# Optimization experiments

Hardware: AMD Instinct MI355X
Metric: run time of the kernel (lower is better)

The kernel has to match this reference:

```python
import jax, jax.numpy as jnp
import numpy as np
import math

L, N, E, H = 2048, 4, 1024, 16  # seq_len, batch, embed_dim, num_heads
HD = E // H                      # head_dim = 64


def setup_inputs() -> dict:
    key = jax.random.key(0)
    ks = jax.random.split(key, 7)
    s = 1.0 / math.sqrt(E)
    return {
        "query": jax.random.normal(ks[0], (L, N, E), jnp.float32),
        "key": jax.random.normal(ks[1], (L, N, E), jnp.float32),
        "value": jax.random.normal(ks[2], (L, N, E), jnp.float32),
        "in_proj_weight": jax.random.normal(ks[3], (3 * E, E), jnp.float32) * s,
        "in_proj_bias": jax.random.normal(ks[4], (3 * E,), jnp.float32) * 0.02,
        "out_proj_weight": jax.random.normal(ks[5], (E, E), jnp.float32) * s,
        "out_proj_bias": jax.random.normal(ks[6], (E,), jnp.float32) * 0.02,
    }


def reference(query, key, value, in_proj_weight, in_proj_bias,
              out_proj_weight, out_proj_bias):
    # --- packed in-projection (q is k is v path of _in_projection_packed) ---
    # F.linear(x, W, b) = x @ W.T + b, W packed as [Wq; Wk; Wv] along dim 0.
    wq, wk, wv = jnp.split(in_proj_weight, 3, axis=0)   # each (E, E)
    bq, bk, bv = jnp.split(in_proj_bias, 3, axis=0)     # each (E,)
    q = query @ wq.T + bq   # (L, N, E)
    k = key @ wk.T + bk
    v = value @ wv.T + bv

    # --- split heads: (L, N, E) -> (N*H, L, HD), matching torch reshape/transpose ---
    def to_heads(x):
        return x.reshape(L, N * H, HD).transpose(1, 0, 2)
    q, k, v = to_heads(q), to_heads(k), to_heads(v)

    # --- scaled dot-product attention (q scaled by 1/sqrt(head_dim)) ---
    q = q / math.sqrt(HD)
    attn = jnp.einsum('bte,bse->bts', q, k)             # (N*H, L, L)
    attn = jax.nn.softmax(attn, axis=-1)
    out = jnp.einsum('bts,bse->bte', attn, v)           # (N*H, L, HD)

    # --- merge heads back to (L, N, E) ---
    out = out.transpose(1, 0, 2).reshape(L, N, E)

    # --- out-projection ---
    out = out @ out_proj_weight.T + out_proj_bias       # (L, N, E)
    return out
```

## Files before the change

kernel.cpp:

```cpp
#include <hip/hip_runtime.h>

using f16 = _Float16;
typedef _Float16 h8 __attribute__((ext_vector_type(8)));
typedef _Float16 h4 __attribute__((ext_vector_type(4)));
typedef float f32x4 __attribute__((ext_vector_type(4)));
typedef float f32x16 __attribute__((ext_vector_type(16)));
typedef unsigned u32x4 __attribute__((ext_vector_type(4)));

constexpr int L_SEQ  = 2048;
constexpr int NBATCH = 4;
constexpr int EMB    = 1024;
constexpr int NHEAD  = 16;
constexpr int HDIM   = 64;
constexpr int BH     = NBATCH * NHEAD;
constexpr int MROWS  = L_SEQ * NBATCH;

#define QSCALE (0.125f * 1.44269504088896341f)

__device__ __forceinline__ void glds16(const void* g, void* l) {
  __builtin_amdgcn_global_load_lds(
      (const __attribute__((address_space(1))) void*)g,
      (__attribute__((address_space(3))) void*)l, 16, 0, 0);
}

__device__ __forceinline__ f32x16 MFMA32(h8 a, h8 b, f32x16 c) {
  return __builtin_amdgcn_mfma_f32_32x32x16_f16(a, b, c, 0, 0, 0);
}
__device__ __forceinline__ unsigned pkrtz(float x, float y) {
  auto t = __builtin_amdgcn_cvt_pkrtz(x, y);
  return __builtin_bit_cast(unsigned, t);
}
__device__ __forceinline__ h8 pack8(f32x4 a, f32x4 b) {
  u32x4 u = { pkrtz(a[0], a[1]), pkrtz(a[2], a[3]),
              pkrtz(b[0], b[1]), pkrtz(b[2], b[3]) };
  return __builtin_bit_cast(h8, u);
}

__global__ __launch_bounds__(256)
void convert_w_kernel(const float* __restrict__ w, const float* __restrict__ wo,
                      f16* __restrict__ wb, f16* __restrict__ wob) {
  const int NW  = 3 * EMB * EMB / 4;
  const int NWO = EMB * EMB / 4;
  const int total = NW + NWO;
  int i = blockIdx.x * blockDim.x + threadIdx.x;
  const int stride = gridDim.x * blockDim.x;
  for (; i < total; i += stride) {
    const float* s; f16* d; int j;
    if (i < NW) { s = w;  d = wb;  j = i;      }
    else        { s = wo; d = wob; j = i - NW; }
    float4 t = reinterpret_cast<const float4*>(s)[j];
    h4 o = { (f16)t.x, (f16)t.y, (f16)t.z, (f16)t.w };
    reinterpret_cast<h4*>(d)[j] = o;
  }
}

__global__ __launch_bounds__(256)
void gemm_qkv(const float* __restrict__ qin, const float* __restrict__ kin,
              const float* __restrict__ vin, const f16* __restrict__ Btbase,
              const float* __restrict__ biasbase, f16* __restrict__ Hbase)
{
  const int id = blockIdx.x;
  const int x   = id & 7;
  const int bnI = (id >> 3) & 7;
  const int bmG = x + 8 * (id >> 6);
  const int z   = bmG >> 6;
  const int bm  = (bmG & 63) * 128;
  const int bn  = bnI * 128;

  const float* A = (z == 0) ? qin : (z == 1) ? kin : vin;
  const f16* Bt = Btbase + (size_t)z * EMB * EMB;
  const float* bias = biasbase + (size_t)z * EMB;

  const int t = threadIdx.x;
  const int w = t >> 6, lane = t & 63;
  const int wr = w >> 1, wc = w & 1;
  const int l16 = lane & 15, g = lane >> 4;

  __shared__ f16 As[2][128][32];
  __shared__ f16 Bs[2][128][32];

  f32x4 acc[4][4] = {};

  const int sr0 = lane >> 2;
  const int sl  = lane & 3;
  const float* gA = &A[(size_t)(bm + w*32 + sr0) * EMB + sl*8];
  const int wslot = 8 * (sl ^ ((sr0 >> 1) & 3));
  f16* lA0 = &As[0][w*32 + sr0][wslot];
  f16* lA0b = &As[0][w*32 + 16 + sr0][wslot];
  const int asStride = 128 * 32;

  const int sr  = lane >> 2;
  const int sc8 = 8 * ((lane & 3) ^ ((lane >> 3) & 3));
  const f16* gB = &Bt[(size_t)(bn + w*32 + sr) * EMB + sc8];

  f32x4 ra0, ra1, rb0, rb1;
  f32x4 sa0, sa1, sb0, sb1;

  ra0 = *(const f32x4*)(gA);
  ra1 = *(const f32x4*)(gA + 4);
  rb0 = *(const f32x4*)(gA + (size_t)16*EMB);
  rb1 = *(const f32x4*)(gA + (size_t)16*EMB + 4);
  *(h8*)lA0  = pack8(ra0, ra1);
  *(h8*)lA0b = pack8(rb0, rb1);
  glds16(gB, &Bs[0][w*32][0]);
  glds16(gB + (size_t)16*EMB, &Bs[0][w*32 + 16][0]);
  sa0 = *(const f32x4*)(gA + 32);
  sa1 = *(const f32x4*)(gA + 36);
  sb0 = *(const f32x4*)(gA + (size_t)16*EMB + 32);
  sb1 = *(const f32x4*)(gA + (size_t)16*EMB + 36);
  glds16(gB + 32, &Bs[1][w*32][0]);
  glds16(gB + (size_t)16*EMB + 32, &Bs[1][w*32 + 16][0]);
  __syncthreads();

  const int fswz = (g ^ ((l16 >> 1) & 3)) * 8;

#pragma unroll 2
  for (int i = 0; i < 32; ++i) {
    const int cur = i & 1;
    if (i < 30) {
      const int k0 = (i + 2) * 32;
      ra0 = *(const f32x4*)(gA + k0);
      ra1 = *(const f32x4*)(gA + k0 + 4);
      rb0 = *(const f32x4*)(gA + (size_t)16*EMB + k0);
      rb1 = *(const f32x4*)(gA + (size_t)16*EMB + k0 + 4);
    }
    if (i < 31) {
      const int k0 = (i + 1) * 32;
      glds16(gB + k0, &Bs[cur ^ 1][w*32][0]);
      glds16(gB + (size_t)16*EMB + k0, &Bs[cur ^ 1][w*32 + 16][0]);
    }

    h8 af[4], bfr[4];
#pragma unroll
    for (int m = 0; m < 4; ++m) af[m]  = *(const h8*)&As[cur][wr*64 + m*16 + l16][fswz];
#pragma unroll
    for (int n = 0; n < 4; ++n) bfr[n] = *(const h8*)&Bs[cur][wc*64 + n*16 + l16][fswz];
    __builtin_amdgcn_s_setprio(1);
#pragma unroll
    for (int m = 0; m < 4; ++m)
#pragma unroll
      for (int n = 0; n < 4; ++n)
        acc[m][n] = __builtin_amdgcn_mfma_f32_16x16x32_f16(af[m], bfr[n], acc[m][n], 0, 0, 0);
    __builtin_amdgcn_s_setprio(0);

    if (i < 31) {
      f16* d0 = lA0  + (cur ^ 1) * asStride;
      f16* d1 = lA0b + (cur ^ 1) * asStride;
      *(h8*)d0 = pack8(sa0, sa1);
      *(h8*)d1 = pack8(sb0, sb1);
      sa0 = ra0; sa1 = ra1; sb0 = rb0; sb1 = rb1;
    }
    __syncthreads();
  }

#pragma unroll
  for (int m = 0; m < 4; ++m) {
#pragma unroll
    for (int n = 0; n < 4; ++n) {
      const int col = bn + wc*64 + n*16 + l16;
      const float bv = bias[col];
#pragma unroll
      for (int r = 0; r < 4; ++r) {
        const int row = bm + wr*64 + m*16 + g*4 + r;
        float v = acc[m][n][r] + bv;
        if (z == 0) v *= QSCALE;
        const int l = row >> 2, nn = row & 3;
        const int h = col >> 6, hd = col & 63;
        Hbase[(((size_t)z * BH + nn * NHEAD + h) * L_SEQ + l) * HDIM + hd] = (f16)v;
      }
    }
  }
}

__global__ __launch_bounds__(256)
void gemm_out(const f16* __restrict__ A, const f16* __restrict__ Bt,
              const float* __restrict__ bias, float* __restrict__ Fout)
{
  const int id = blockIdx.x;
  const int x   = id & 7;
  const int bnI = (id >> 3) & 7;
  const int bmG = x + 8 * (id >> 6);
  const int bm  = bmG * 128;
  const int bn  = bnI * 128;

  const int t = threadIdx.x;
  const int w = t >> 6, lane = t & 63;
  const int wr = w >> 1, wc = w & 1;
  const int l16 = lane & 15, g = lane >> 4;

  __shared__ f16 As[2][128][32];
  __shared__ f16 Bs[2][128][32];

  f32x4 acc[4][4] = {};

  const int sr  = lane >> 2;
  const int sc8 = 8 * ((lane & 3) ^ ((lane >> 3) & 3));
  const f16* gA = &A [(size_t)(bm + w*32 + sr) * EMB + sc8];
  const f16* gB = &Bt[(size_t)(bn + w*32 + sr) * EMB + sc8];

  glds16(gA, &As[0][w*32][0]);
  glds16(gA + (size_t)16*EMB, &As[0][w*32 + 16][0]);
  glds16(gB, &Bs[0][w*32][0]);
  glds16(gB + (size_t)16*EMB, &Bs[0][w*32 + 16][0]);
  __syncthreads();

  const int fswz = (g ^ ((l16 >> 1) & 3)) * 8;

#pragma unroll 1
  for (int i = 0; i < 32; ++i) {
    const int cur = i & 1;
    if (i < 31) {
      const int k0 = (i + 1) * 32;
      glds16(gA + k0, &As[cur ^ 1][w*32][0]);
      glds16(gA + (size_t)16*EMB + k0, &As[cur ^ 1][w*32 + 16][0]);
      glds16(gB + k0, &Bs[cur ^ 1][w*32][0]);
      glds16(gB + (size_t)16*EMB + k0, &Bs[cur ^ 1][w*32 + 16][0]);
    }

    h8 af[4], bfr[4];
#pragma unroll
    for (int m = 0; m < 4; ++m) af[m]  = *(const h8*)&As[cur][wr*64 + m*16 + l16][fswz];
#pragma unroll
    for (int n = 0; n < 4; ++n) bfr[n] = *(const h8*)&Bs[cur][wc*64 + n*16 + l16][fswz];
    __builtin_amdgcn_s_setprio(1);
#pragma unroll
    for (int m = 0; m < 4; ++m)
#pragma unroll
      for (int n = 0; n < 4; ++n)
        acc[m][n] = __builtin_amdgcn_mfma_f32_16x16x32_f16(af[m], bfr[n], acc[m][n], 0, 0, 0);
    __builtin_amdgcn_s_setprio(0);
    __syncthreads();
  }

#pragma unroll
  for (int m = 0; m < 4; ++m) {
#pragma unroll
    for (int n = 0; n < 4; ++n) {
      const int col = bn + wc*64 + n*16 + l16;
      const float bv = bias[col];
#pragma unroll
      for (int r = 0; r < 4; ++r) {
        const int row = bm + wr*64 + m*16 + g*4 + r;
        Fout[(size_t)row * EMB + col] = acc[m][n][r] + bv;
      }
    }
  }
}

__global__ __launch_bounds__(256)
void vtrans_kernel(const f16* __restrict__ V, f16* __restrict__ Vt) {
  const int b = blockIdx.y;
  const int t = threadIdx.x;
  const int d = t & 63;
  const int l0 = (blockIdx.x * 4 + (t >> 6)) * 8;
  const f16* Vb = V  + (size_t)b * L_SEQ * HDIM;
  f16* Vtb      = Vt + (size_t)b * L_SEQ * HDIM;
  h8 v;
#pragma unroll
  for (int i = 0; i < 8; ++i) v[i] = Vb[(size_t)(l0 + i) * HDIM + d];
  *(h8*)&Vtb[(size_t)d * L_SEQ + l0] = v;
}

__device__ __forceinline__ void attn11_step(
    const f16* __restrict__ Kc, const f16* __restrict__ Vc,
    const h8 (&qf)[4],
    f32x16 (&o)[2], float (&psum)[4],
    int l31, int hi)
{
  const int swz = (l31 & 7) << 3;

  h8 pa[4];
#pragma unroll
  for (int kt = 0; kt < 2; ++kt) {
    f32x16 acc = {};
    __builtin_amdgcn_s_setprio(1);
#pragma unroll
    for (int s = 0; s < 4; ++s) {
      h8 kf = *(const h8*)&Kc[(kt*32 + l31)*64 + ((s*16 + hi*8) ^ swz)];
      acc = MFMA32(kf, qf[s], acc);
    }
    __builtin_amdgcn_s_setprio(0);

#pragma unroll
    for (int half = 0; half < 2; ++half) {
      float p0 = __builtin_amdgcn_exp2f(acc[half*8+0]);
      float p1 = __builtin_amdgcn_exp2f(acc[half*8+1]);
      float p2 = __builtin_amdgcn_exp2f(acc[half*8+2]);
      float p3 = __builtin_amdgcn_exp2f(acc[half*8+3]);
      float p4 = __builtin_amdgcn_exp2f(acc[half*8+4]);
      float p5 = __builtin_amdgcn_exp2f(acc[half*8+5]);
      float p6 = __builtin_amdgcn_exp2f(acc[half*8+6]);
      float p7 = __builtin_amdgcn_exp2f(acc[half*8+7]);
      psum[0] += p0 + p4;
      psum[1] += p1 + p5;
      psum[2] += p2 + p6;
      psum[3] += p3 + p7;
      unsigned A = pkrtz(p0, p1);
      unsigned C = pkrtz(p2, p3);
      unsigned B = pkrtz(p4, p5);
      unsigned D = pkrtz(p6, p7);
      asm("v_permlane32_swap_b32 %0, %1" : "+v"(A), "+v"(B));
      asm("v_permlane32_swap_b32 %0, %1" : "+v"(C), "+v"(D));
      u32x4 wv = { A, C, B, D };
      pa[kt*2 + half] = __builtin_bit_cast(h8, wv);
    }
  }

#pragma unroll
  for (int s2 = 0; s2 < 4; ++s2) {
    h8 vf0 = *(const h8*)&Vc[(0*32 + l31)*64 + ((s2*16 + hi*8) ^ swz)];
    h8 vf1 = *(const h8*)&Vc[(1*32 + l31)*64 + ((s2*16 + hi*8) ^ swz)];
    __builtin_amdgcn_s_setprio(1);
    o[0] = MFMA32(pa[s2], vf0, o[0]);
    o[1] = MFMA32(pa[s2], vf1, o[1]);
    __builtin_amdgcn_s_setprio(0);
  }
}

__global__ __launch_bounds__(256, 4)
void attn11_kernel(const f16* __restrict__ Qh, const f16* __restrict__ Kh,
                   const f16* __restrict__ Vt, f16* __restrict__ AO)
{
  const int id = blockIdx.x;
  const int b    = (id & 7) | ((id >> 7) << 3);
  const int qblk = (id >> 3) & 15;

  const int t = threadIdx.x;
  const int w = t >> 6, lane = t & 63;
  const int l31 = lane & 31, hi = lane >> 5;

  const f16* Qb = Qh + (size_t)b * L_SEQ * HDIM;
  const f16* Kb = Kh + (size_t)b * L_SEQ * HDIM;
  const f16* Vb = Vt + (size_t)b * (size_t)HDIM * L_SEQ;

  __shared__ f16 Ks[2][64*64];
  __shared__ f16 Vs[2][64*64];

  const int q0 = qblk * 128 + w * 32;

  h8 qf[4];
#pragma unroll
  for (int s = 0; s < 4; ++s)
    qf[s] = *(const h8*)&Qb[(size_t)(q0 + l31) * HDIM + s*16 + hi*8];

  const int srow = lane >> 3;
  const int scol = 8 * ((lane & 7) ^ srow);
  const int r0   = w*16 + srow;
  const f16* gK0 = Kb + (size_t)(r0    ) * HDIM + scol;
  const f16* gK1 = Kb + (size_t)(r0 + 8) * HDIM + scol;
  const f16* gV0 = Vb + (size_t)(r0    ) * L_SEQ + scol;
  const f16* gV1 = Vb + (size_t)(r0 + 8) * L_SEQ + scol;
  const int ldsw = w * 1024;

  f32x16 o[2] = {};
  float psum[4] = { 0.f, 0.f, 0.f, 0.f };

  glds16(gK0, &Ks[0][ldsw]);
  glds16(gK1, &Ks[0][ldsw + 512]);
  glds16(gV0, &Vs[0][ldsw]);
  glds16(gV1, &Vs[0][ldsw + 512]);
  __syncthreads();

#pragma unroll 1
  for (int j0 = 0; j0 < L_SEQ; j0 += 128) {
    {
      const int jn = (j0 + 64) & (L_SEQ - 1);
      glds16(gK0 + (size_t)jn * HDIM, &Ks[1][ldsw]);
      glds16(gK1 + (size_t)jn * HDIM, &Ks[1][ldsw + 512]);
      glds16(gV0 + jn, &Vs[1][ldsw]);
      glds16(gV1 + jn, &Vs[1][ldsw + 512]);
      attn11_step(&Ks[0][0], &Vs[0][0], qf, o, psum, l31, hi);
      __syncthreads();
    }
    {
      const int jn = (j0 + 128) & (L_SEQ - 1);
      glds16(gK0 + (size_t)jn * HDIM, &Ks[0][ldsw]);
      glds16(gK1 + (size_t)jn * HDIM, &Ks[0][ldsw + 512]);
      glds16(gV0 + jn, &Vs[0][ldsw]);
      glds16(gV1 + jn, &Vs[0][ldsw + 512]);
      attn11_step(&Ks[1][0], &Vs[1][0], qf, o, psum, l31, hi);
      __syncthreads();
    }
  }

  float ssum = (psum[0] + psum[1]) + (psum[2] + psum[3]);
  ssum += __shfl_xor(ssum, 32);
  const float inv = 1.0f / ssum;

  const int nn = b >> 4, h = b & 15;
#pragma unroll
  for (int r = 0; r < 16; ++r) {
    const int qrow = (r & 3) + 8 * (r >> 2) + 4 * hi;
    const float iv = __shfl(inv, qrow);
    const int lr = q0 + qrow;
#pragma unroll
    for (int dt = 0; dt < 2; ++dt)
      AO[((size_t)lr * NBATCH + nn) * EMB + h*HDIM + dt*32 + l31] =
          (f16)(o[dt][r] * iv);
  }
}

extern "C" void kernel_launch(void* const* d_in, const int* in_sizes, int n_in,
                              void* d_out, int out_size, void* d_ws, size_t ws_size,
                              hipStream_t stream) {
  const float* query = (const float*)d_in[0];
  const float* key   = (const float*)d_in[1];
  const float* value = (const float*)d_in[2];
  const float* in_w  = (const float*)d_in[3];
  const float* in_b  = (const float*)d_in[4];
  const float* out_w = (const float*)d_in[5];
  const float* out_b = (const float*)d_in[6];
  float* out = (float*)d_out;

  char* ws = (char*)d_ws;
  size_t offH  = 0;
  size_t offX  = offH  + (size_t)3 * BH * L_SEQ * HDIM * 2;
  size_t offW  = offX  + (size_t)3 * MROWS * EMB * 2;
  size_t offWo = offW  + (size_t)3 * EMB * EMB * 2;
  size_t offAO = offWo + (size_t)EMB * EMB * 2;
  f16* Hbase = (f16*)(ws + offH);
  f16* Xb    = (f16*)(ws + offX);
  f16* Wb    = (f16*)(ws + offW);
  f16* Wob   = (f16*)(ws + offWo);
  f16* AOb   = (f16*)(ws + offAO);
  f16* Vtb   = Xb;

  hipLaunchKernelGGL(convert_w_kernel, dim3(1024), dim3(256), 0, stream,
                     in_w, out_w, Wb, Wob);

  hipLaunchKernelGGL(gemm_qkv, dim3(1536), dim3(256), 0, stream,
                     query, key, value, Wb, in_b, Hbase);

  f16* Vh = Hbase + (size_t)2 * BH * L_SEQ * HDIM;
  hipLaunchKernelGGL(vtrans_kernel, dim3(L_SEQ/32, BH), dim3(256), 0, stream, Vh, Vtb);

  hipLaunchKernelGGL(attn11_kernel, dim3(L_SEQ/128 * BH), dim3(256), 0, stream,
                     Hbase,
                     Hbase + (size_t)BH * L_SEQ * HDIM,
                     Vtb, AOb);

  hipLaunchKernelGGL(gemm_out, dim3(512), dim3(256), 0, stream,
                     AOb, Wob, out_b, out);
}
```

Measured before the change: 212.6 us.

## Process two 32-row query tiles per wave to reuse K/V fragments

The attention kernel now has each wave handle two query tiles (256 query rows per block instead of 128). Each K and V fragment read from LDS therefore feeds twice as many MFMAs, and the grid is halved. This cuts LDS traffic and global K/V loads per unit of work and gives the scheduler more independent MFMA chains to interleave with exp. In exchange it doubles accumulator and Q registers, lowers the occupancy target to 2 blocks per SIMD group, and leaves fewer blocks in flight (512).

```diff
diff --git a/kernel.cpp b/kernel.cpp
--- a/kernel.cpp
+++ b/kernel.cpp
@@ -261,49 +261,63 @@
   *(h8*)&Vtb[(size_t)d * L_SEQ + l0] = v;
 }
 
-__device__ __forceinline__ void attn11_step(
+__device__ __forceinline__ void expack(const f32x16& acc, float (&ps)[4],
+                                       h8& paA, h8& paB) {
+#pragma unroll
+  for (int half = 0; half < 2; ++half) {
+    float p0 = __builtin_amdgcn_exp2f(acc[half*8+0]);
+    float p1 = __builtin_amdgcn_exp2f(acc[half*8+1]);
+    float p2 = __builtin_amdgcn_exp2f(acc[half*8+2]);
+    float p3 = __builtin_amdgcn_exp2f(acc[half*8+3]);
+    float p4 = __builtin_amdgcn_exp2f(acc[half*8+4]);
+    float p5 = __builtin_amdgcn_exp2f(acc[half*8+5]);
+    float p6 = __builtin_amdgcn_exp2f(acc[half*8+6]);
+    float p7 = __builtin_amdgcn_exp2f(acc[half*8+7]);
+    ps[0] += p0 + p4;
+    ps[1] += p1 + p5;
+    ps[2] += p2 + p6;
+    ps[3] += p3 + p7;
+    unsigned A = pkrtz(p0, p1);
+    unsigned C = pkrtz(p2, p3);
+    unsigned B = pkrtz(p4, p5);
+    unsigned D = pkrtz(p6, p7);
+    asm("v_permlane32_swap_b32 %0, %1" : "+v"(A), "+v"(B));
+    asm("v_permlane32_swap_b32 %0, %1" : "+v"(C), "+v"(D));
+    u32x4 wv = { A, C, B, D };
+    h8 r = __builtin_bit_cast(h8, wv);
+    if (half == 0) paA = r; else paB = r;
+  }
+}
+
+__device__ __forceinline__ void attn12_step(
     const f16* __restrict__ Kc, const f16* __restrict__ Vc,
-    const h8 (&qf)[4],
-    f32x16 (&o)[2], float (&psum)[4],
+    const h8 (&qf0)[4], const h8 (&qf1)[4],
+    f32x16 (&o0)[2], f32x16 (&o1)[2],
+    float (&ps0)[4], float (&ps1)[4],
     int l31, int hi)
 {
   const int swz = (l31 & 7) << 3;
 
-  h8 pa[4];
+  h8 pa0[4], pa1[4];
 #pragma unroll
   for (int kt = 0; kt < 2; ++kt) {
-    f32x16 acc = {};
+    h8 kf[4];
+#pragma unroll
+    for (int s = 0; s < 4; ++s)
+      kf[s] = *(const h8*)&Kc[(kt*32 + l31)*64 + ((s*16 + hi*8) ^ swz)];
+
+    f32x16 acc0 = {};
+    f32x16 acc1 = {};
     __builtin_amdgcn_s_setprio(1);
 #pragma unroll
     for (int s = 0; s < 4; ++s) {
-      h8 kf = *(const h8*)&Kc[(kt*32 + l31)*64 + ((s*16 + hi*8) ^ swz)];
-      acc = MFMA32(kf, qf[s], acc);
+      acc0 = MFMA32(kf[s], qf0[s], acc0);
+      acc1 = MFMA32(kf[s], qf1[s], acc1);
     }
     __builtin_amdgcn_s_setprio(0);
 
-#pragma unroll
-    for (int half = 0; half < 2; ++half) {
-      float p0 = __builtin_amdgcn_exp2f(acc[half*8+0]);
-      float p1 = __builtin_amdgcn_exp2f(acc[half*8+1]);
-      float p2 = __builtin_amdgcn_exp2f(acc[half*8+2]);
-      float p3 = __builtin_amdgcn_exp2f(acc[half*8+3]);
-      float p4 = __builtin_amdgcn_exp2f(acc[half*8+4]);
-      float p5 = __builtin_amdgcn_exp2f(acc[half*8+5]);
-      float p6 = __builtin_amdgcn_exp2f(acc[half*8+6]);
-      float p7 = __builtin_amdgcn_exp2f(acc[half*8+7]);
-      psum[0] += p0 + p4;
-      psum[1] += p1 + p5;
-      psum[2] += p2 + p6;
-      psum[3] += p3 + p7;
-      unsigned A = pkrtz(p0, p1);
-      unsigned C = pkrtz(p2, p3);
-      unsigned B = pkrtz(p4, p5);
-      unsigned D = pkrtz(p6, p7);
-      asm("v_permlane32_swap_b32 %0, %1" : "+v"(A), "+v"(B));
-      asm("v_permlane32_swap_b32 %0, %1" : "+v"(C), "+v"(D));
-      u32x4 wv = { A, C, B, D };
-      pa[kt*2 + half] = __builtin_bit_cast(h8, wv);
-    }
+    expack(acc0, ps0, pa0[kt*2], pa0[kt*2+1]);
+    expack(acc1, ps1, pa1[kt*2], pa1[kt*2+1]);
   }
 
 #pragma unroll
@@ -311,19 +325,21 @@
     h8 vf0 = *(const h8*)&Vc[(0*32 + l31)*64 + ((s2*16 + hi*8) ^ swz)];
     h8 vf1 = *(const h8*)&Vc[(1*32 + l31)*64 + ((s2*16 + hi*8) ^ swz)];
     __builtin_amdgcn_s_setprio(1);
-    o[0] = MFMA32(pa[s2], vf0, o[0]);
-    o[1] = MFMA32(pa[s2], vf1, o[1]);
+    o0[0] = MFMA32(pa0[s2], vf0, o0[0]);
+    o0[1] = MFMA32(pa0[s2], vf1, o0[1]);
+    o1[0] = MFMA32(pa1[s2], vf0, o1[0]);
+    o1[1] = MFMA32(pa1[s2], vf1, o1[1]);
     __builtin_amdgcn_s_setprio(0);
   }
 }
 
-__global__ __launch_bounds__(256, 4)
-void attn11_kernel(const f16* __restrict__ Qh, const f16* __restrict__ Kh,
+__global__ __launch_bounds__(256, 2)
+void attn12_kernel(const f16* __restrict__ Qh, const f16* __restrict__ Kh,
                    const f16* __restrict__ Vt, f16* __restrict__ AO)
 {
   const int id = blockIdx.x;
-  const int b    = (id & 7) | ((id >> 7) << 3);
-  const int qblk = (id >> 3) & 15;
+  const int b    = (id & 7) | ((id >> 6) << 3);
+  const int qblk = (id >> 3) & 7;
 
   const int t = threadIdx.x;
   const int w = t >> 6, lane = t & 63;
@@ -336,12 +352,14 @@
   __shared__ f16 Ks[2][64*64];
   __shared__ f16 Vs[2][64*64];
 
-  const int q0 = qblk * 128 + w * 32;
-
-  h8 qf[4];
-#pragma unroll
-  for (int s = 0; s < 4; ++s)
-    qf[s] = *(const h8*)&Qb[(size_t)(q0 + l31) * HDIM + s*16 + hi*8];
+  const int q0 = qblk * 256 + w * 32;
+
+  h8 qf0[4], qf1[4];
+#pragma unroll
+  for (int s = 0; s < 4; ++s) {
+    qf0[s] = *(const h8*)&Qb[(size_t)(q0 + l31) * HDIM + s*16 + hi*8];
+    qf1[s] = *(const h8*)&Qb[(size_t)(q0 + 128 + l31) * HDIM + s*16 + hi*8];
+  }
 
   const int srow = lane >> 3;
   const int scol = 8 * ((lane & 7) ^ srow);
@@ -352,8 +370,10 @@
   const f16* gV1 = Vb + (size_t)(r0 + 8) * L_SEQ + scol;
   const int ldsw = w * 1024;
 
-  f32x16 o[2] = {};
-  float psum[4] = { 0.f, 0.f, 0.f, 0.f };
+  f32x16 o0[2] = {};
+  f32x16 o1[2] = {};
+  float ps0[4] = { 0.f, 0.f, 0.f, 0.f };
+  float ps1[4] = { 0.f, 0.f, 0.f, 0.f };
 
   glds16(gK0, &Ks[0][ldsw]);
   glds16(gK1, &Ks[0][ldsw + 512]);
@@ -369,7 +389,7 @@
       glds16(gK1 + (size_t)jn * HDIM, &Ks[1][ldsw + 512]);
       glds16(gV0 + jn, &Vs[1][ldsw]);
       glds16(gV1 + jn, &Vs[1][ldsw + 512]);
-      attn11_step(&Ks[0][0], &Vs[0][0], qf, o, psum, l31, hi);
+      attn12_step(&Ks[0][0], &Vs[0][0], qf0, qf1, o0, o1, ps0, ps1, l31, hi);
       __syncthreads();
     }
     {
@@ -378,25 +398,38 @@
       glds16(gK1 + (size_t)jn * HDIM, &Ks[0][ldsw + 512]);
       glds16(gV0 + jn, &Vs[0][ldsw]);
       glds16(gV1 + jn, &Vs[0][ldsw + 512]);
-      attn11_step(&Ks[1][0], &Vs[1][0], qf, o, psum, l31, hi);
+      attn12_step(&Ks[1][0], &Vs[1][0], qf0, qf1, o0, o1, ps0, ps1, l31, hi);
       __syncthreads();
     }
   }
 
-  float ssum = (psum[0] + psum[1]) + (psum[2] + psum[3]);
-  ssum += __shfl_xor(ssum, 32);
-  const float inv = 1.0f / ssum;
-
   const int nn = b >> 4, h = b & 15;
+  float ssum0 = (ps0[0] + ps0[1]) + (ps0[2] + ps0[3]);
+  ssum0 += __shfl_xor(ssum0, 32);
+  const float inv0 = 1.0f / ssum0;
+  float ssum1 = (ps1[0] + ps1[1]) + (ps1[2] + ps1[3]);
+  ssum1 += __shfl_xor(ssum1, 32);
+  const float inv1 = 1.0f / ssum1;
+
 #pragma unroll
   for (int r = 0; r < 16; ++r) {
     const int qrow = (r & 3) + 8 * (r >> 2) + 4 * hi;
-    const float iv = __shfl(inv, qrow);
-    const int lr = q0 + qrow;
-#pragma unroll
-    for (int dt = 0; dt < 2; ++dt)
-      AO[((size_t)lr * NBATCH + nn) * EMB + h*HDIM + dt*32 + l31] =
-          (f16)(o[dt][r] * iv);
+    {
+      const float iv = __shfl(inv0, qrow);
+      const int lr = q0 + qrow;
+#pragma unroll
+      for (int dt = 0; dt < 2; ++dt)
+        AO[((size_t)lr * NBATCH + nn) * EMB + h*HDIM + dt*32 + l31] =
+            (f16)(o0[dt][r] * iv);
+    }
+    {
+      const float iv = __shfl(inv1, qrow);
+      const int lr = q0 + 128 + qrow;
+#pragma unroll
+      for (int dt = 0; dt < 2; ++dt)
+        AO[((size_t)lr * NBATCH + nn) * EMB + h*HDIM + dt*32 + l31] =
+            (f16)(o1[dt][r] * iv);
+    }
   }
 }
 
@@ -434,7 +467,7 @@
   f16* Vh = Hbase + (size_t)2 * BH * L_SEQ * HDIM;
   hipLaunchKernelGGL(vtrans_kernel, dim3(L_SEQ/32, BH), dim3(256), 0, stream, Vh, Vtb);
 
-  hipLaunchKernelGGL(attn11_kernel, dim3(L_SEQ/128 * BH), dim3(256), 0, stream,
+  hipLaunchKernelGGL(attn12_kernel, dim3(512), dim3(256), 0, stream,
                      Hbase,
                      Hbase + (size_t)BH * L_SEQ * HDIM,
                      Vtb, AOb);
```

Result: faster. 207.8 us, median of 3 (-2.2%).
